# Kernel tuning notes

Measured on AMD Instinct MI355X. Metric: run time of the kernel, lower is better.

The kernel has to match this reference:

```python
import jax, jax.numpy as jnp
import numpy as np

# config constants (match init_kwargs)
C = 1024
NH = 16
HS = C // NH
CHUNK = 64          # attn_chunk_size
TOPK = 32           # attn_topk
WINDOW = 4096       # kv_cache_window_size
MIN_KV = 16384      # min_kv_cache_size
MAX_KV = 32768      # max_kv_cache_size
SHORT = 4096        # short_sequence_criteria
CT = 65536          # incoming kv-cache length


def setup_inputs() -> dict:
    key = jax.random.key(0)
    ks = jax.random.split(key, 7)
    s = 1.0 / np.sqrt(C)
    return {
        "x": jax.random.normal(ks[0], (C,), jnp.float32),
        "k_cache": jax.random.normal(ks[1], (1, CT, C), jnp.float32),
        "v_cache": jax.random.normal(ks[2], (1, CT, C), jnp.float32),
        "Wr": jax.random.normal(ks[3], (C, C), jnp.float32) * s,
        "Wk": jax.random.normal(ks[4], (C, C), jnp.float32) * s,
        "Wv": jax.random.normal(ks[5], (C, C), jnp.float32) * s,
        "Wo": jax.random.normal(ks[6], (C, C), jnp.float32) * s,
    }


def _split_heads(t):  # (1, T, C) -> (1, NH, T, HS)
    return t.reshape(1, t.shape[1], NH, HS).transpose(0, 2, 1, 3)


def _update_kv_cache(q, k_cache, v_cache):
    # q: (1,1,C); caches: (1,CT,C). CT > MIN_KV so compression runs.
    past = CT - WINDOW
    kp = _split_heads(k_cache[:, :past])          # (1,NH,past,HS)
    vp = _split_heads(v_cache[:, :past])
    qh = _split_heads(q)                          # (1,NH,1,HS)
    scores = jnp.einsum("bhqd,bhkd->bhqk", qh, kp) / np.sqrt(HS)
    w = jax.nn.softmax(scores, axis=-1)           # (1,NH,1,past)
    vote = w.sum(axis=-2)                         # (1,NH,past)
    keep = MIN_KV - WINDOW                        # per-head tokens kept
    _, idx = jax.lax.top_k(vote, keep)            # (1,NH,keep), descending vote order
    kpc = jnp.take_along_axis(kp, idx[..., None], axis=2)  # (1,NH,keep,HS)
    vpc = jnp.take_along_axis(vp, idx[..., None], axis=2)
    kpc = kpc.transpose(0, 2, 1, 3).reshape(1, keep, C)
    vpc = vpc.transpose(0, 2, 1, 3).reshape(1, keep, C)
    k_new = jnp.concatenate([kpc, k_cache[:, past:]], axis=1)  # (1, MIN_KV, C)
    v_new = jnp.concatenate([vpc, v_cache[:, past:]], axis=1)
    return k_new, v_new


def reference(x, k_cache, v_cache, Wr, Wk, Wv, Wo):
    x2 = x[None, None, :]                         # (1,1,C)
    q = x2 @ Wr.T
    k = x2 @ Wk.T
    v = x2 @ Wv.T

    # CT > MAX_KV -> compress cache (eviction via attention vote per head)
    k_cache, v_cache = _update_kv_cache(q, k_cache, v_cache)
    CT2 = k_cache.shape[1]                        # MIN_KV = 16384 > SHORT -> sparse path

    num_chunks = CT2 // CHUNK
    kc = k_cache.reshape(1, num_chunks, CHUNK, C)
    vc = v_cache.reshape(1, num_chunks, CHUNK, C)
    chunk_key = kc.mean(axis=2)                   # (1,num_chunks,C)
    chunk_score = jnp.einsum("bqc,bkc->bqk", q, chunk_key)
    _, tidx = jax.lax.top_k(chunk_score[0, 0], TOPK)  # (TOPK,)
    topk_k = kc[:, tidx].reshape(1, TOPK * CHUNK, C)
    topk_v = vc[:, tidx].reshape(1, TOPK * CHUNK, C)

    k_comb = jnp.concatenate([topk_k, k], axis=1)  # (1, TOPK*CHUNK+1, C)
    v_comb = jnp.concatenate([topk_v, v], axis=1)

    qh = _split_heads(q)                          # (1,NH,1,HS)
    kh = _split_heads(k_comb)
    vh = _split_heads(v_comb)
    attn = jax.nn.softmax(
        jnp.einsum("bhqd,bhkd->bhqk", qh, kh) / np.sqrt(HS), axis=-1)
    y = jnp.einsum("bhqk,bhkd->bhqd", attn, vh)   # (1,NH,1,HS)
    y = y.transpose(0, 2, 1, 3).reshape(C)
    y = y @ Wo.T
    return y
```

## Files before the change

kernel.cpp:

```cpp
#include <hip/hip_runtime.h>
#include <stdint.h>

#define C      1024
#define NH     16
#define HS     64
#define CT     65536
#define PAST   61440
#define KEEP   12288
#define NCOMP  192
#define NSEL   32
#define NB     8192
#define NBLK   256

typedef unsigned long long ull;

#define LD_A(p)   __hip_atomic_load((p), __ATOMIC_RELAXED, __HIP_MEMORY_SCOPE_AGENT)
#define ST_A(p,v) __hip_atomic_store((p), (v), __ATOMIC_RELAXED, __HIP_MEMORY_SCOPE_AGENT)

__device__ __forceinline__ unsigned int desc_key(float f) {
    unsigned int b = __float_as_uint(f);
    return (b >> 31) ? b : (~b & 0x7FFFFFFFu);
}
__device__ __forceinline__ float u_to_f(unsigned int u) {
    unsigned int b = (u & 0x80000000u) ? u : (0x7FFFFFFFu - u);
    return __uint_as_float(b);
}
__device__ __forceinline__ int bin_of(float s, float hi, float scale) {
    int b = (int)((hi - s) * scale);
    return b < 0 ? 0 : (b > NB - 1 ? NB - 1 : b);
}
__device__ __forceinline__ void load_params(const unsigned* umin, const unsigned* umax,
                                            int h, float* hi, float* sc) {
    float h2 = u_to_f(umin[h]);
    float lo = u_to_f(umax[h]);
    float r = h2 - lo;
    *hi = h2;
    *sc = (r > 0.f) ? (float)(NB - 1) / r : 0.f;
}

__device__ __forceinline__ void gsync(unsigned* bar, int site) {
    __syncthreads();
    if (threadIdx.x == 0) {
        asm volatile("s_waitcnt vmcnt(0)" ::: "memory");
        unsigned* g    = bar + site * 288 + (blockIdx.x >> 5) * 32;
        unsigned* root = bar + site * 288 + 256;
        if (__hip_atomic_fetch_add(g, 1u, __ATOMIC_RELAXED, __HIP_MEMORY_SCOPE_AGENT) == 31u)
            __hip_atomic_fetch_add(root, 1u, __ATOMIC_RELAXED, __HIP_MEMORY_SCOPE_AGENT);
        while (LD_A(root) < 8u) __builtin_amdgcn_s_sleep(16);
    }
    __syncthreads();
}
__device__ __forceinline__ void hsync(unsigned* bar, int site, int h) {
    __syncthreads();
    if (threadIdx.x == 0) {
        asm volatile("s_waitcnt vmcnt(0)" ::: "memory");
        unsigned* c = bar + 576 + (site * 16 + h) * 32;
        __hip_atomic_fetch_add(c, 1u, __ATOMIC_RELAXED, __HIP_MEMORY_SCOPE_AGENT);
        while (LD_A(c) < 16u) __builtin_amdgcn_s_sleep(8);
    }
    __syncthreads();
}

__global__ void k_proj(const float* __restrict__ x, const float* __restrict__ Wr,
                       const float* __restrict__ Wk, const float* __restrict__ Wv,
                       float* __restrict__ q, float* __restrict__ kn, float* __restrict__ vn,
                       unsigned* __restrict__ hc, unsigned* __restrict__ umin,
                       unsigned* __restrict__ umax, ull* __restrict__ cs_fix,
                       unsigned* __restrict__ bar) {
    int gid = blockIdx.x * 256 + threadIdx.x;
    for (int i = gid; i < 2 * NH * NB; i += 196608) hc[i] = 0;
    if (blockIdx.x >= 512 && blockIdx.x < 520)
        bar[(blockIdx.x - 512) * 256 + threadIdx.x] = 0u;
    if (blockIdx.x == 700) {
        if (threadIdx.x < 16) umin[threadIdx.x] = 0xFFFFFFFFu;
        else if (threadIdx.x < 32) umax[threadIdx.x - 16] = 0u;
    }
    if (blockIdx.x == 701 && threadIdx.x < 256) cs_fix[threadIdx.x] = 0ull;

    int w = blockIdx.x * (blockDim.x >> 6) + (threadIdx.x >> 6);
    int lane = threadIdx.x & 63;
    int mat = w >> 10, row = w & 1023;
    const float* W = (mat == 0) ? Wr : (mat == 1) ? Wk : Wv;
    const float4* Wrow = (const float4*)(W + (size_t)row * C);
    const float4* x4 = (const float4*)x;
    float acc = 0.f;
#pragma unroll
    for (int i = 0; i < 4; ++i) {
        float4 a = Wrow[i * 64 + lane];
        float4 b = x4[i * 64 + lane];
        acc += a.x * b.x + a.y * b.y + a.z * b.z + a.w * b.w;
    }
#pragma unroll
    for (int off = 32; off; off >>= 1) acc += __shfl_xor(acc, off);
    if (lane == 0) { (mat == 0 ? q : (mat == 1 ? kn : vn))[row] = acc; }
}

__global__ void k_scores(const float* __restrict__ kc, const float* __restrict__ q,
                         float* __restrict__ s, unsigned* __restrict__ umin,
                         unsigned* __restrict__ umax, ull* __restrict__ cs_fix) {
    __shared__ float sc_l[4][16][17];
    __shared__ float smn[4][16], smx[4][16];
    __shared__ long long wred[4];
    int wave = threadIdx.x >> 6, lane = threadIdx.x & 63;
    int wid = blockIdx.x * 4 + wave;
    int t0 = wid * 16;
    const float4* q4 = (const float4*)q;
    float4 qv[4];
#pragma unroll
    for (int i = 0; i < 4; ++i) qv[i] = q4[i * 64 + lane];
    float mnv[4] = {3.4e38f, 3.4e38f, 3.4e38f, 3.4e38f};
    float mxv[4] = {-3.4e38f, -3.4e38f, -3.4e38f, -3.4e38f};
    for (int tt = 0; tt < 16; ++tt) {
        const float4* row = (const float4*)(kc + (size_t)(t0 + tt) * C);
        float acc[4];
#pragma unroll
        for (int i = 0; i < 4; ++i) {
            float4 a = row[i * 64 + lane];
            acc[i] = a.x * qv[i].x + a.y * qv[i].y + a.z * qv[i].z + a.w * qv[i].w;
        }
#pragma unroll
        for (int off = 8; off; off >>= 1) {
#pragma unroll
            for (int i = 0; i < 4; ++i) acc[i] += __shfl_xor(acc[i], off);
        }
        if ((lane & 15) == 0) {
            int g = lane >> 4;
#pragma unroll
            for (int i = 0; i < 4; ++i) {
                sc_l[wave][4 * i + g][tt] = acc[i];
                mnv[i] = fminf(mnv[i], acc[i]);
                mxv[i] = fmaxf(mxv[i], acc[i]);
            }
        }
    }
    __syncthreads();
    int tt2 = lane & 15;
#pragma unroll
    for (int r = 0; r < 4; ++r) {
        int h = r * 4 + (lane >> 4);
        s[(size_t)h * CT + t0 + tt2] = sc_l[wave][h][tt2];
    }
    if (blockIdx.x < 960) {
        if ((lane & 15) == 0) {
            int g = lane >> 4;
#pragma unroll
            for (int i = 0; i < 4; ++i) { smn[wave][4 * i + g] = mnv[i]; smx[wave][4 * i + g] = mxv[i]; }
        }
        __syncthreads();
        if (threadIdx.x < 16) {
            int h = threadIdx.x;
            float mn = smn[0][h], mx = smx[0][h];
            for (int w2 = 1; w2 < 4; ++w2) {
                mn = fminf(mn, smn[w2][h]);
                mx = fmaxf(mx, smx[w2][h]);
            }
            atomicMin(&umin[h], desc_key(mx));
            atomicMax(&umax[h], desc_key(mn));
        }
    } else {
        int hh = threadIdx.x >> 4, tt = threadIdx.x & 15;
        long long f = 0;
#pragma unroll
        for (int w2 = 0; w2 < 4; ++w2) f += llrintf(sc_l[w2][hh][tt] * 16777216.f);
#pragma unroll
        for (int off = 32; off; off >>= 1) f += __shfl_xor(f, off);
        if (lane == 0) wred[wave] = f;
        __syncthreads();
        if (threadIdx.x == 0)
            cs_fix[NCOMP + (blockIdx.x - 960)] =
                (ull)(wred[0] + wred[1] + wred[2] + wred[3]);
    }
}

__global__ __launch_bounds__(1024, 2) void k_mega(
        const float* __restrict__ s, const float* __restrict__ vc,
        const unsigned* __restrict__ umin, const unsigned* __restrict__ umax,
        unsigned* __restrict__ hist, unsigned* __restrict__ cnt,
        ull* __restrict__ G, unsigned* __restrict__ stok,
        ull* __restrict__ cs_fix, float* __restrict__ part,
        const float* __restrict__ q, const float* __restrict__ kn,
        const float* __restrict__ vn, const float* __restrict__ Wo,
        float* __restrict__ out, unsigned* __restrict__ bar) {
    const int bid = blockIdx.x, tid = threadIdx.x;
    const int lane = tid & 63, wave = tid >> 6;
    const int h = bid >> 4, seg = bid & 15;
    __shared__ __align__(16) char smem[40960];
    __shared__ unsigned shT, shN;
    __shared__ unsigned wsum[16];

    float hi, sc; load_params(umin, umax, h, &hi, &sc);
    unsigned* lh = (unsigned*)smem;

    {
        for (int i = tid; i < NB; i += 1024) lh[i] = 0;
        __syncthreads();
        const float* sh = s + (size_t)h * CT + seg * 3840;
        for (int i = tid; i < 3840; i += 1024)
            atomicAdd(&lh[bin_of(sh[i], hi, sc)], 1u);
        __syncthreads();
        unsigned* gh = hist + h * NB;
        for (int i = tid; i < NB; i += 1024) {
            unsigned c = lh[i];
            if (c) atomicAdd(&gh[i], c);
        }
    }
    hsync(bar, 0, h);

    {
        const unsigned* gh = hist + h * NB;
        unsigned c8[8]; unsigned loc = 0; int b0 = tid * 8;
#pragma unroll
        for (int k = 0; k < 8; ++k) { c8[k] = gh[b0 + k]; loc += c8[k]; }
        unsigned run = loc;
#pragma unroll
        for (int off = 1; off < 64; off <<= 1) {
            unsigned n = __shfl_up(run, off);
            if (lane >= off) run += n;
        }
        if (lane == 63) wsum[wave] = run;
        __syncthreads();
        if (wave == 0 && lane < 16) {
            unsigned v = wsum[lane];
#pragma unroll
            for (int off = 1; off < 16; off <<= 1) {
                unsigned n = __shfl_up(v, off);
                if (lane >= off) v += n;
            }
            wsum[lane] = v;
        }
        __syncthreads();
        unsigned r = run - loc + (wave ? wsum[wave - 1] : 0u);
#pragma unroll
        for (int k = 0; k < 8; ++k) {
            unsigned c = c8[k];
            lh[b0 + k] = r;
            unsigned inc = r + c;
            if (r < KEEP && inc >= KEEP) { shT = (unsigned)(b0 + k); shN = inc; }
            r = inc;
        }
    }
    __syncthreads();
    const unsigned T = shT, ncand = shN;

    {
        const float* sh = s + (size_t)h * CT + seg * 3840;
        unsigned* ch = cnt + h * NB;
        ull* Gh = G + (size_t)h * 65536;
        for (int i = tid; i < 3840; i += 1024) {
            float v = sh[i];
            int b = bin_of(v, hi, sc);
            if ((unsigned)b <= T) {
                unsigned pos = lh[b] + atomicAdd(&ch[b], 1u);
                ST_A(&Gh[pos], ((ull)desc_key(v) << 16) | (unsigned)(seg * 3840 + i));
            }
        }
    }
    hsync(bar, 1, h);

    {
        ull* csl = (ull*)(smem + 32768);
        if (tid < NCOMP) csl[tid] = 0ull;
        __syncthreads();
        const ull* Gh = G + (size_t)h * 65536;
        for (unsigned p = seg * 1024 + tid; p < ncand; p += 16384) {
            ull pk = Gh[p];
            unsigned u = (unsigned)(pk >> 16);
            float v = u_to_f(u);
            int b = bin_of(v, hi, sc);
            unsigned start = lh[b];
            unsigned end = (b == NB - 1) ? ncand : lh[b + 1];
            unsigned rank = start;
            for (unsigned j = start; j < end; ++j) rank += (Gh[j] < pk) ? 1u : 0u;
            if (rank < KEEP) {
                ST_A(&stok[h * KEEP + rank], (unsigned)(pk & 0xFFFFull));
                long long f = llrintf(v * 16777216.f);
                atomicAdd(&csl[rank >> 6], (ull)f);
            }
        }
        __syncthreads();
        if (tid < NCOMP) {
            ull c = csl[tid];
            if (c) atomicAdd(&cs_fix[tid], c);
        }
    }
    gsync(bar, 0);

    {
        ull* key = (ull*)smem;
        unsigned* sel_l = (unsigned*)(smem + 2048);
        float* scm = (float*)(smem + 2176);
        float* exb = (float*)(smem + 2688);
        float* vbuf = (float*)(smem + 3200);
        if (tid < 256) {
            long long v = (long long)cs_fix[tid];
            ull bb = (ull)(v + (1ll << 45));
            key[tid] = (((1ull << 46) - bb) << 8) | (unsigned)tid;
        }
        __syncthreads();
        for (unsigned k = 2; k <= 256; k <<= 1) {
            for (unsigned j = k >> 1; j > 0; j >>= 1) {
                if (tid < 256) {
                    unsigned ixj = tid ^ j;
                    if (ixj > (unsigned)tid) {
                        ull a = key[tid], b = key[ixj];
                        bool up = ((tid & k) == 0);
                        if (up ? (a > b) : (a < b)) { key[tid] = b; key[ixj] = a; }
                    }
                }
                __syncthreads();
            }
        }
        if (tid < NSEL) sel_l[tid] = (unsigned)(key[tid] & 0xFFull);
        __syncthreads();

        int su = tid >> 9, sid = tid & 511;
        int p = bid * 2 + su;
        int hh = p >> 5, ci = p & 31;
        int c = (int)sel_l[ci];
        int g = sid >> 3, q8 = sid & 7;
        int t = (c < NCOMP) ? (int)stok[hh * KEEP + c * 64 + g]
                            : (PAST + (c - NCOMP) * 64 + g);
        if (q8 == 0) scm[su * 64 + g] = s[(size_t)hh * CT + t] * 0.125f;
        __syncthreads();
        float m = -1e30f;
        for (int j = 0; j < 64; ++j) m = fmaxf(m, scm[su * 64 + j]);
        float e = expf(scm[su * 64 + g] - m);
        if (q8 == 0) exb[su * 64 + g] = e;
        const float4* vrow = (const float4*)(vc + (size_t)t * C + hh * HS);
        float4 v0 = vrow[q8 * 2], v1 = vrow[q8 * 2 + 1];
        float* vb = vbuf + su * 4352 + g * 68 + q8 * 8;
        vb[0] = e * v0.x; vb[1] = e * v0.y; vb[2] = e * v0.z; vb[3] = e * v0.w;
        vb[4] = e * v1.x; vb[5] = e * v1.y; vb[6] = e * v1.z; vb[7] = e * v1.w;
        __syncthreads();
        if (sid < 64) {
            float acc = 0.f;
            for (int g2 = 0; g2 < 64; ++g2) acc += vbuf[su * 4352 + g2 * 68 + sid];
            float* P = part + (size_t)(hh * 32 + ci) * 68;
            ST_A(&P[2 + sid], acc);
            if (sid == 0) {
                float es = 0.f;
                for (int g2 = 0; g2 < 64; ++g2) es += exb[su * 64 + g2];
                ST_A(&P[0], m);
                ST_A(&P[1], es);
            }
        }
    }
    gsync(bar, 1);
    if (bid >= 64) return;

    {
        float* yl = (float*)smem;
        float* qdl = (float*)(smem + 4096);
        if (tid < 16) {
            float qd = 0.f;
            for (int l = 0; l < 64; ++l) qd += q[tid * 64 + l] * kn[tid * 64 + l];
            qdl[tid] = qd;
        }
        __syncthreads();
        {
            int hh = tid >> 6, ln = tid & 63;
            float a_new = qdl[hh] * 0.125f;
            const float* P0 = part + (size_t)hh * 32 * 68;
            float m = a_new;
            for (int ci = 0; ci < 32; ++ci) m = fmaxf(m, P0[ci * 68]);
            float den = expf(a_new - m);
            float acc = den * vn[hh * HS + ln];
            for (int ci = 0; ci < 32; ++ci) {
                float w = expf(P0[ci * 68] - m);
                den += w * P0[ci * 68 + 1];
                acc += w * P0[ci * 68 + 2 + ln];
            }
            yl[tid] = acc / den;
        }
        __syncthreads();
        int r = bid * 16 + wave;
        const float4* Wrow = (const float4*)(Wo + (size_t)r * C);
        const float4* y4 = (const float4*)yl;
        float acc = 0.f;
#pragma unroll
        for (int i = 0; i < 4; ++i) {
            float4 a = Wrow[i * 64 + lane];
            float4 b = y4[i * 64 + lane];
            acc += a.x * b.x + a.y * b.y + a.z * b.z + a.w * b.w;
        }
#pragma unroll
        for (int off = 32; off; off >>= 1) acc += __shfl_xor(acc, off);
        if (lane == 0) out[r] = acc;
    }
}

extern "C" void kernel_launch(void* const* d_in, const int* in_sizes, int n_in,
                              void* d_out, int out_size, void* d_ws, size_t ws_size,
                              hipStream_t stream) {
    const float* x  = (const float*)d_in[0];
    const float* kc = (const float*)d_in[1];
    const float* vc = (const float*)d_in[2];
    const float* Wr = (const float*)d_in[3];
    const float* Wk = (const float*)d_in[4];
    const float* Wv = (const float*)d_in[5];
    const float* Wo = (const float*)d_in[6];
    float* out = (float*)d_out;
    char* ws = (char*)d_ws;

    float* q    = (float*)(ws + 0);
    float* kn   = (float*)(ws + 8192);
    float* vn   = (float*)(ws + 16384);
    ull* cs_fix = (ull*)(ws + 32768);
    float* part = (float*)(ws + 49152);
    unsigned* stok = (unsigned*)(ws + 196608);
    unsigned* umin = (unsigned*)(ws + 1048576);
    unsigned* umax = (unsigned*)(ws + 1048640);
    unsigned* bar  = (unsigned*)(ws + 1048832);
    unsigned* hist = (unsigned*)(ws + 1114112);
    unsigned* cnt  = (unsigned*)(ws + 1638400);
    float* s = (float*)(ws + 2621440);
    ull* G = (ull*)(ws + 7340032);

    k_proj<<<768, 256, 0, stream>>>(x, Wr, Wk, Wv, q, kn, vn, hist, umin, umax, cs_fix, bar);
    k_scores<<<1024, 256, 0, stream>>>(kc, q, s, umin, umax, cs_fix);
    k_mega<<<NBLK, 1024, 0, stream>>>(s, vc, umin, umax, hist, cnt, G, stok, cs_fix,
                                      part, q, kn, vn, Wo, out, bar);
}
```

Baseline: 130.4 us.

## Replace atomic-counter grid barriers with per-block phase flags and distribute final projection

New measurement: 124.0 us. -5.0%, faster.

```diff
diff --git a/kernel.cpp b/kernel.cpp
--- a/kernel.cpp
+++ b/kernel.cpp
@@ -11,6 +11,7 @@
 #define NSEL   32
 #define NB     8192
 #define NBLK   256
+#define FLAGW  8
 
 typedef unsigned long long ull;
 
@@ -38,26 +39,23 @@
     *sc = (r > 0.f) ? (float)(NB - 1) / r : 0.f;
 }
 
-__device__ __forceinline__ void gsync(unsigned* bar, int site) {
+__device__ __forceinline__ void arrive(unsigned* flag, unsigned ph) {
     __syncthreads();
     if (threadIdx.x == 0) {
         asm volatile("s_waitcnt vmcnt(0)" ::: "memory");
-        unsigned* g    = bar + site * 288 + (blockIdx.x >> 5) * 32;
-        unsigned* root = bar + site * 288 + 256;
-        if (__hip_atomic_fetch_add(g, 1u, __ATOMIC_RELAXED, __HIP_MEMORY_SCOPE_AGENT) == 31u)
-            __hip_atomic_fetch_add(root, 1u, __ATOMIC_RELAXED, __HIP_MEMORY_SCOPE_AGENT);
-        while (LD_A(root) < 8u) __builtin_amdgcn_s_sleep(16);
-    }
+        ST_A(&flag[blockIdx.x * FLAGW], ph);
+    }
+}
+__device__ __forceinline__ void wait_head(unsigned* flag, unsigned ph, int h) {
+    if (threadIdx.x < 16)
+        while (LD_A(&flag[(h * 16 + threadIdx.x) * FLAGW]) < ph)
+            __builtin_amdgcn_s_sleep(2);
     __syncthreads();
 }
-__device__ __forceinline__ void hsync(unsigned* bar, int site, int h) {
-    __syncthreads();
-    if (threadIdx.x == 0) {
-        asm volatile("s_waitcnt vmcnt(0)" ::: "memory");
-        unsigned* c = bar + 576 + (site * 16 + h) * 32;
-        __hip_atomic_fetch_add(c, 1u, __ATOMIC_RELAXED, __HIP_MEMORY_SCOPE_AGENT);
-        while (LD_A(c) < 16u) __builtin_amdgcn_s_sleep(8);
-    }
+__device__ __forceinline__ void wait_all(unsigned* flag, unsigned ph) {
+    if (threadIdx.x < 256)
+        while (LD_A(&flag[threadIdx.x * FLAGW]) < ph)
+            __builtin_amdgcn_s_sleep(2);
     __syncthreads();
 }
 
@@ -66,11 +64,11 @@
                        float* __restrict__ q, float* __restrict__ kn, float* __restrict__ vn,
                        unsigned* __restrict__ hc, unsigned* __restrict__ umin,
                        unsigned* __restrict__ umax, ull* __restrict__ cs_fix,
-                       unsigned* __restrict__ bar) {
+                       unsigned* __restrict__ flag) {
     int gid = blockIdx.x * 256 + threadIdx.x;
     for (int i = gid; i < 2 * NH * NB; i += 196608) hc[i] = 0;
     if (blockIdx.x >= 512 && blockIdx.x < 520)
-        bar[(blockIdx.x - 512) * 256 + threadIdx.x] = 0u;
+        flag[(blockIdx.x - 512) * 256 + threadIdx.x] = 0u;
     if (blockIdx.x == 700) {
         if (threadIdx.x < 16) umin[threadIdx.x] = 0xFFFFFFFFu;
         else if (threadIdx.x < 32) umax[threadIdx.x - 16] = 0u;
@@ -180,7 +178,8 @@
         ull* __restrict__ cs_fix, float* __restrict__ part,
         const float* __restrict__ q, const float* __restrict__ kn,
         const float* __restrict__ vn, const float* __restrict__ Wo,
-        float* __restrict__ out, unsigned* __restrict__ bar) {
+        float* __restrict__ yg, float* __restrict__ out,
+        unsigned* __restrict__ flag) {
     const int bid = blockIdx.x, tid = threadIdx.x;
     const int lane = tid & 63, wave = tid >> 6;
     const int h = bid >> 4, seg = bid & 15;
@@ -204,7 +203,7 @@
             if (c) atomicAdd(&gh[i], c);
         }
     }
-    hsync(bar, 0, h);
+    arrive(flag, 1); wait_head(flag, 1, h);
 
     {
         const unsigned* gh = hist + h * NB;
@@ -255,7 +254,7 @@
             }
         }
     }
-    hsync(bar, 1, h);
+    arrive(flag, 2); wait_head(flag, 2, h);
 
     {
         ull* csl = (ull*)(smem + 32768);
@@ -283,7 +282,7 @@
             if (c) atomicAdd(&cs_fix[tid], c);
         }
     }
-    gsync(bar, 0);
+    arrive(flag, 3); wait_all(flag, 3);
 
     {
         ull* key = (ull*)smem;
@@ -345,47 +344,43 @@
             }
         }
     }
-    gsync(bar, 1);
-    if (bid >= 64) return;
+    arrive(flag, 4); wait_head(flag, 4, h);
+
+    if (seg == 0 && tid < 64) {
+        float p = q[h * 64 + tid] * kn[h * 64 + tid];
+#pragma unroll
+        for (int off = 32; off; off >>= 1) p += __shfl_xor(p, off);
+        float a_new = p * 0.125f;
+        const float* P0 = part + (size_t)h * 32 * 68;
+        float m = a_new;
+        for (int ci = 0; ci < 32; ++ci) m = fmaxf(m, P0[ci * 68]);
+        float den = expf(a_new - m);
+        float acc = den * vn[h * HS + tid];
+        for (int ci = 0; ci < 32; ++ci) {
+            float w = expf(P0[ci * 68] - m);
+            den += w * P0[ci * 68 + 1];
+            acc += w * P0[ci * 68 + 2 + tid];
+        }
+        ST_A(&yg[h * HS + tid], acc / den);
+    }
+    arrive(flag, 5); wait_all(flag, 5);
 
     {
         float* yl = (float*)smem;
-        float* qdl = (float*)(smem + 4096);
-        if (tid < 16) {
-            float qd = 0.f;
-            for (int l = 0; l < 64; ++l) qd += q[tid * 64 + l] * kn[tid * 64 + l];
-            qdl[tid] = qd;
-        }
-        __syncthreads();
-        {
-            int hh = tid >> 6, ln = tid & 63;
-            float a_new = qdl[hh] * 0.125f;
-            const float* P0 = part + (size_t)hh * 32 * 68;
-            float m = a_new;
-            for (int ci = 0; ci < 32; ++ci) m = fmaxf(m, P0[ci * 68]);
-            float den = expf(a_new - m);
-            float acc = den * vn[hh * HS + ln];
-            for (int ci = 0; ci < 32; ++ci) {
-                float w = expf(P0[ci * 68] - m);
-                den += w * P0[ci * 68 + 1];
-                acc += w * P0[ci * 68 + 2 + ln];
-            }
-            yl[tid] = acc / den;
-        }
-        __syncthreads();
-        int r = bid * 16 + wave;
-        const float4* Wrow = (const float4*)(Wo + (size_t)r * C);
-        const float4* y4 = (const float4*)yl;
-        float acc = 0.f;
-#pragma unroll
-        for (int i = 0; i < 4; ++i) {
-            float4 a = Wrow[i * 64 + lane];
-            float4 b = y4[i * 64 + lane];
-            acc += a.x * b.x + a.y * b.y + a.z * b.z + a.w * b.w;
-        }
+        float* ps = (float*)(smem + 4096);
+        yl[tid] = yg[tid];
+        __syncthreads();
+        int row = bid * 4 + (wave >> 2), qtr = wave & 3;
+        const float4* Wrow = (const float4*)(Wo + (size_t)row * C) + qtr * 64;
+        const float4* y4 = (const float4*)yl + qtr * 64;
+        float4 a = Wrow[lane], b = y4[lane];
+        float acc = a.x * b.x + a.y * b.y + a.z * b.z + a.w * b.w;
 #pragma unroll
         for (int off = 32; off; off >>= 1) acc += __shfl_xor(acc, off);
-        if (lane == 0) out[r] = acc;
+        if (lane == 0) ps[wave] = acc;
+        __syncthreads();
+        if (tid < 4)
+            out[bid * 4 + tid] = ps[tid * 4] + ps[tid * 4 + 1] + ps[tid * 4 + 2] + ps[tid * 4 + 3];
     }
 }
 
@@ -406,18 +401,19 @@
     float* kn   = (float*)(ws + 8192);
     float* vn   = (float*)(ws + 16384);
     ull* cs_fix = (ull*)(ws + 32768);
+    float* yg   = (float*)(ws + 40960);
     float* part = (float*)(ws + 49152);
     unsigned* stok = (unsigned*)(ws + 196608);
     unsigned* umin = (unsigned*)(ws + 1048576);
     unsigned* umax = (unsigned*)(ws + 1048640);
-    unsigned* bar  = (unsigned*)(ws + 1048832);
+    unsigned* flag = (unsigned*)(ws + 1048832);
     unsigned* hist = (unsigned*)(ws + 1114112);
     unsigned* cnt  = (unsigned*)(ws + 1638400);
     float* s = (float*)(ws + 2621440);
     ull* G = (ull*)(ws + 7340032);
 
-    k_proj<<<768, 256, 0, stream>>>(x, Wr, Wk, Wv, q, kn, vn, hist, umin, umax, cs_fix, bar);
+    k_proj<<<768, 256, 0, stream>>>(x, Wr, Wk, Wv, q, kn, vn, hist, umin, umax, cs_fix, flag);
     k_scores<<<1024, 256, 0, stream>>>(kc, q, s, umin, umax, cs_fix);
     k_mega<<<NBLK, 1024, 0, stream>>>(s, vc, umin, umax, hist, cnt, G, stok, cs_fix,
-                                      part, q, kn, vn, Wo, out, bar);
-}
+                                      part, q, kn, vn, Wo, yg, out, flag);
+}
```
